# Performance work log

Hardware: AMD Instinct MI355X
Metric: run time of the kernel (lower is better)

## Reference

```python
import jax, jax.numpy as jnp
import numpy as np

HEADS = 8
DIM_HEAD = 64
SCALE = DIM_HEAD ** -0.5


def setup_inputs() -> dict:
    key = jax.random.key(0)
    ks = jax.random.split(key, 6)
    b, n, d_model = 16, 1024, 512
    inner = HEADS * DIM_HEAD  # 512
    std = d_model ** -0.5
    return {
        "x": jax.random.normal(ks[0], (b, n, d_model), jnp.float32),
        "Wq": jax.random.normal(ks[1], (inner, d_model), jnp.float32) * std,
        "Wk": jax.random.normal(ks[2], (inner, d_model), jnp.float32) * std,
        "Wv": jax.random.normal(ks[3], (inner, d_model), jnp.float32) * std,
        "rel_bias": jax.random.normal(ks[4], (HEADS, n, n), jnp.float32) * 0.02,
        "Wo": jax.random.normal(ks[5], (d_model, inner), jnp.float32) * std,
        "bo": jnp.zeros((d_model,), jnp.float32),
    }


def reference(x, Wq, Wk, Wv, rel_bias, Wo, bo):
    b, n, _ = x.shape
    # projections (Linear with weight of shape [out, in], no bias)
    def proj_heads(W):
        t = jnp.einsum('bnc,ec->bne', x, W)             # [b, n, inner]
        return t.reshape(b, n, HEADS, DIM_HEAD).transpose(0, 2, 1, 3)  # [b, h, n, d]
    q = proj_heads(Wq)
    k = proj_heads(Wk)
    v = proj_heads(Wv)
    sim = jnp.einsum('bhid,bhjd->bhij', q, k) * SCALE
    sim = sim + rel_bias[None]                          # additive rel-pos bias
    attn = jax.nn.softmax(sim, axis=-1)
    out = jnp.einsum('bhij,bhjd->bhid', attn, v)        # [b, h, n, d]
    out = out.transpose(0, 2, 1, 3).reshape(b, n, HEADS * DIM_HEAD)
    return jnp.einsum('bne,ce->bnc', out, Wo) + bo
```

## Files before the change

### kernel.cpp

```cpp
#include <hip/hip_runtime.h>

typedef unsigned short u16;
typedef short short8 __attribute__((ext_vector_type(8)));
typedef float fx4 __attribute__((ext_vector_type(4)));
typedef u16 u16x4 __attribute__((ext_vector_type(4)));
typedef u16 u16x8 __attribute__((ext_vector_type(8)));


__device__ __forceinline__ u16 f2bf(float f) {
  union { float f; unsigned u; } v; v.f = f;
  unsigned r = (v.u + 0x7fffu + ((v.u >> 16) & 1u)) >> 16;
  return (u16)r;
}
__device__ __forceinline__ float bf2f(u16 u) {
  union { unsigned u; float f; } v; v.u = ((unsigned)u) << 16;
  return v.f;
}
__device__ __forceinline__ void load_lds16(const void* g, void* l) {
  __builtin_amdgcn_global_load_lds((const __attribute__((address_space(1))) void*)g,
                                   (__attribute__((address_space(3))) void*)l, 16, 0, 0);
}
__device__ __forceinline__ int swz(int row, int colb) {
  return (row << 7) | (colb ^ ((row & 7) << 4));
}

__global__ __launch_bounds__(256) void k_convert(
    const float* __restrict__ x, const float* __restrict__ wq, const float* __restrict__ wk,
    const float* __restrict__ wv, const float* __restrict__ wo, const float* __restrict__ bias,
    u16* __restrict__ xb, u16* __restrict__ wqkv, u16* __restrict__ wob, u16* __restrict__ biasb) {
  const int total = 2228224;
  for (int u = blockIdx.x * blockDim.x + threadIdx.x; u < total; u += gridDim.x * blockDim.x) {
    const float* src; u16* dst; int off;
    if (u < 1048576)      { src = x;    dst = xb;            off = u << 3; }
    else if (u < 1081344) { src = wq;   dst = wqkv;          off = (u - 1048576) << 3; }
    else if (u < 1114112) { src = wk;   dst = wqkv + 262144; off = (u - 1081344) << 3; }
    else if (u < 1146880) { src = wv;   dst = wqkv + 524288; off = (u - 1114112) << 3; }
    else if (u < 1179648) { src = wo;   dst = wob;           off = (u - 1146880) << 3; }
    else                  { src = bias; dst = biasb;         off = (u - 1179648) << 3; }
    float4 a = *(const float4*)(src + off);
    float4 b = *(const float4*)(src + off + 4);
    u16x8 o;
    o[0] = f2bf(a.x); o[1] = f2bf(a.y); o[2] = f2bf(a.z); o[3] = f2bf(a.w);
    o[4] = f2bf(b.x); o[5] = f2bf(b.y); o[6] = f2bf(b.z); o[7] = f2bf(b.w);
    *(u16x8*)(dst + off) = o;
  }
}

__device__ __forceinline__ void gemm_core(const u16* __restrict__ A, const u16* __restrict__ Bm,
                                          int mt, int nt, int tid, fx4 acc[4][4],
                                          u16* ldsA, u16* ldsB) {
  const int w = tid >> 6, l = tid & 63;
  const int wr = w >> 1, wc = w & 1;
  const int lr = l & 15, kg = (l >> 4) * 8;
  for (int k0 = 0; k0 < 512; k0 += 32) {
#pragma unroll
    for (int i = 0; i < 2; ++i) {
      int seg = w * 2 + i;
      int idx = seg * 512 + l * 8;
      int row = idx >> 5, col = idx & 31;
      load_lds16(A  + (mt * 128 + row) * 512 + k0 + col, (char*)ldsA + seg * 1024);
      load_lds16(Bm + (nt * 128 + row) * 512 + k0 + col, (char*)ldsB + seg * 1024);
    }
    __syncthreads();
    short8 a[4], b[4];
#pragma unroll
    for (int mi = 0; mi < 4; ++mi) a[mi] = *(const short8*)&ldsA[(wr * 64 + mi * 16 + lr) * 32 + kg];
#pragma unroll
    for (int ni = 0; ni < 4; ++ni) b[ni] = *(const short8*)&ldsB[(wc * 64 + ni * 16 + lr) * 32 + kg];
#pragma unroll
    for (int mi = 0; mi < 4; ++mi)
#pragma unroll
      for (int ni = 0; ni < 4; ++ni)
        acc[mi][ni] = __builtin_amdgcn_mfma_f32_16x16x32_bf16(a[mi], b[ni], acc[mi][ni], 0, 0, 0);
    __syncthreads();
  }
}

__global__ __launch_bounds__(256) void k_proj(const u16* __restrict__ xb, const u16* __restrict__ wqkv,
                                              u16* __restrict__ Qb, u16* __restrict__ Kb,
                                              u16* __restrict__ Vtb) {
  __shared__ u16 ldsA[128 * 32], ldsB[128 * 32];
  int orig = blockIdx.x;
  int wgid = (orig & 7) * 192 + (orig >> 3);
  int mt = wgid / 12, nt = wgid % 12;
  int tid = threadIdx.x;
  fx4 acc[4][4] = {};
  gemm_core(xb, wqkv, mt, nt, tid, acc, ldsA, ldsB);
  const int w = tid >> 6, l = tid & 63, wr = w >> 1, wc = w & 1;
  const int rb = mt * 128 + wr * 64 + ((l >> 4) << 2);
  const int eb = ((nt & 3) << 7) + wc * 64 + (l & 15);
  if (nt < 8) {
    u16* dst = (nt < 4) ? Qb : Kb;
#pragma unroll
    for (int ni = 0; ni < 4; ++ni) {
      int e = eb + ni * 16, hh = e >> 6, d = e & 63;
#pragma unroll
      for (int mi = 0; mi < 4; ++mi)
#pragma unroll
        for (int j = 0; j < 4; ++j) {
          int r = rb + mi * 16 + j, bb = r >> 10, nn = r & 1023;
          dst[(((bb << 3) + hh) * 1024 + nn) * 64 + d] = f2bf(acc[mi][ni][j]);
        }
    }
  } else {
#pragma unroll
    for (int ni = 0; ni < 4; ++ni) {
      int e = eb + ni * 16, hh = e >> 6, d = e & 63;
#pragma unroll
      for (int mi = 0; mi < 4; ++mi) {
        int r0 = rb + mi * 16, bb = r0 >> 10, nn = r0 & 1023;
        u16x4 p;
#pragma unroll
        for (int j = 0; j < 4; ++j) p[j] = f2bf(acc[mi][ni][j]);
        *(u16x4*)&Vtb[(((bb << 3) + hh) * 64 + d) * 1024 + nn] = p;
      }
    }
  }
}

__global__ __launch_bounds__(256) void k_attn(const u16* __restrict__ Qb, const u16* __restrict__ Kb,
                                              const u16* __restrict__ Vtb, const u16* __restrict__ biasb,
                                              u16* __restrict__ Ob) {
  __shared__ u16 ldsK[64 * 64], ldsV[64 * 64], ldsBias[64 * 64];
  __shared__ u16 ldsP[4][16 * 64];
  int orig = blockIdx.x;
  int wgid = (orig & 7) * 256 + (orig >> 3);
  int h = wgid >> 8, bb = (wgid >> 4) & 15, qt = wgid & 15;
  const int tid = threadIdx.x, w = tid >> 6, l = tid & 63;
  const int lr = l & 15, g = l >> 4;
  const int q0 = qt * 64;
  const u16*  Qbh = Qb + (size_t)((bb * 8 + h) * 1024) * 64;
  const char* Kc  = (const char*)(Kb  + (size_t)((bb * 8 + h) * 1024) * 64);
  const char* Vc  = (const char*)(Vtb + (size_t)((bb * 8 + h) * 64) * 1024);
  const char* Bc  = (const char*)biasb + ((size_t)h << 21);
  const int qrow = q0 + w * 16 + lr;
  short8 qf0 = *(const short8*)&Qbh[qrow * 64 + g * 8];
  short8 qf1 = *(const short8*)&Qbh[qrow * 64 + 32 + g * 8];
  float m_r[4], l_r[4];
  fx4 acc_o[4] = {};
#pragma unroll
  for (int j = 0; j < 4; ++j) { m_r[j] = -1e30f; l_r[j] = 0.f; }

  for (int kt = 0; kt < 16; ++kt) {
#pragma unroll
    for (int i = 0; i < 2; ++i) {
      int segb = (w * 2 + i) * 1024;
      int o = segb + l * 16;
      int bs = o ^ (((o >> 7) & 7) << 4);
      int row = bs >> 7, colb = bs & 127;
      load_lds16(Kc + (size_t)(kt * 64 + row) * 128 + colb, (char*)ldsK + segb);
      load_lds16(Vc + (size_t)row * 2048 + kt * 128 + colb, (char*)ldsV + segb);
      load_lds16(Bc + (size_t)(q0 + row) * 2048 + kt * 128 + colb, (char*)ldsBias + segb);
    }
    __syncthreads();
    fx4 s[4];
#pragma unroll
    for (int ct = 0; ct < 4; ++ct) {
      short8 kf0 = *(const short8*)((char*)ldsK + swz(ct * 16 + lr, g * 16));
      short8 kf1 = *(const short8*)((char*)ldsK + swz(ct * 16 + lr, 64 + g * 16));
      fx4 t = {};
      t = __builtin_amdgcn_mfma_f32_16x16x32_bf16(qf0, kf0, t, 0, 0, 0);
      t = __builtin_amdgcn_mfma_f32_16x16x32_bf16(qf1, kf1, t, 0, 0, 0);
      s[ct] = t;
    }
#pragma unroll
    for (int ct = 0; ct < 4; ++ct)
#pragma unroll
      for (int j = 0; j < 4; ++j) {
        u16 bv = *(const u16*)((char*)ldsBias + swz(w * 16 + g * 4 + j, (ct * 16 + lr) * 2));
        s[ct][j] = s[ct][j] * 0.125f + bf2f(bv);
      }
#pragma unroll
    for (int j = 0; j < 4; ++j) {
      float tm = fmaxf(fmaxf(s[0][j], s[1][j]), fmaxf(s[2][j], s[3][j]));
#pragma unroll
      for (int d = 1; d < 16; d <<= 1) tm = fmaxf(tm, __shfl_xor(tm, d));
      float mn = fmaxf(m_r[j], tm);
      float corr = __expf(m_r[j] - mn);
      m_r[j] = mn;
      float rs = 0.f;
#pragma unroll
      for (int ct = 0; ct < 4; ++ct) { float p = __expf(s[ct][j] - mn); s[ct][j] = p; rs += p; }
#pragma unroll
      for (int d = 1; d < 16; d <<= 1) rs += __shfl_xor(rs, d);
      l_r[j] = l_r[j] * corr + rs;
#pragma unroll
      for (int dt = 0; dt < 4; ++dt) acc_o[dt][j] *= corr;
    }
    char* Pw = (char*)ldsP[w];
#pragma unroll
    for (int ct = 0; ct < 4; ++ct)
#pragma unroll
      for (int j = 0; j < 4; ++j)
        *(u16*)(Pw + swz(g * 4 + j, (ct * 16 + lr) * 2)) = f2bf(s[ct][j]);
    __syncthreads();
    short8 pf0 = *(const short8*)(Pw + swz(lr, g * 16));
    short8 pf1 = *(const short8*)(Pw + swz(lr, 64 + g * 16));
#pragma unroll
    for (int dt = 0; dt < 4; ++dt) {
      short8 vf0 = *(const short8*)((char*)ldsV + swz(dt * 16 + lr, g * 16));
      short8 vf1 = *(const short8*)((char*)ldsV + swz(dt * 16 + lr, 64 + g * 16));
      acc_o[dt] = __builtin_amdgcn_mfma_f32_16x16x32_bf16(pf0, vf0, acc_o[dt], 0, 0, 0);
      acc_o[dt] = __builtin_amdgcn_mfma_f32_16x16x32_bf16(pf1, vf1, acc_o[dt], 0, 0, 0);
    }
    __syncthreads();
  }
#pragma unroll
  for (int j = 0; j < 4; ++j) {
    float inv = 1.f / l_r[j];
    int q = q0 + w * 16 + g * 4 + j;
#pragma unroll
    for (int dt = 0; dt < 4; ++dt) {
      int col = h * 64 + dt * 16 + lr;
      Ob[(size_t)(bb * 1024 + q) * 512 + col] = f2bf(acc_o[dt][j] * inv);
    }
  }
}

__global__ __launch_bounds__(256) void k_out(const u16* __restrict__ Ob, const u16* __restrict__ Wob,
                                             const float* __restrict__ bo, float* __restrict__ out) {
  __shared__ u16 ldsA[128 * 32], ldsB[128 * 32];
  int orig = blockIdx.x;
  int wgid = (orig & 7) * 64 + (orig >> 3);
  int mt = wgid >> 2, nt = wgid & 3;
  int tid = threadIdx.x;
  fx4 acc[4][4] = {};
  gemm_core(Ob, Wob, mt, nt, tid, acc, ldsA, ldsB);
  const int w = tid >> 6, l = tid & 63, wr = w >> 1, wc = w & 1;
  const int rb = mt * 128 + wr * 64 + ((l >> 4) << 2);
  const int eb = nt * 128 + wc * 64 + (l & 15);
#pragma unroll
  for (int ni = 0; ni < 4; ++ni) {
    int e = eb + ni * 16;
    float bv = bo[e];
#pragma unroll
    for (int mi = 0; mi < 4; ++mi)
#pragma unroll
      for (int j = 0; j < 4; ++j) {
        int r = rb + mi * 16 + j;
        out[(size_t)r * 512 + e] = acc[mi][ni][j] + bv;
      }
  }
}

extern "C" void kernel_launch(void* const* d_in, const int* in_sizes, int n_in,
                              void* d_out, int out_size, void* d_ws, size_t ws_size,
                              hipStream_t stream) {
  const float* x    = (const float*)d_in[0];
  const float* wq   = (const float*)d_in[1];
  const float* wk   = (const float*)d_in[2];
  const float* wv   = (const float*)d_in[3];
  const float* bias = (const float*)d_in[4];
  const float* wo   = (const float*)d_in[5];
  const float* bo   = (const float*)d_in[6];
  float* out = (float*)d_out;
  char* ws = (char*)d_ws;
  u16* xb    = (u16*)(ws + 0);
  u16* wqkv  = (u16*)(ws + 16777216);
  u16* wob   = (u16*)(ws + 18350080);
  u16* biasb = (u16*)(ws + 18874368);
  u16* Qb    = (u16*)(ws + 35651584);
  u16* Kb    = (u16*)(ws + 52428800);
  u16* Vtb   = (u16*)(ws + 69206016);
  u16* Ob    = (u16*)(ws + 85983232);

  hipLaunchKernelGGL(k_convert, dim3(2048), dim3(256), 0, stream,
                     x, wq, wk, wv, wo, bias, xb, wqkv, wob, biasb);
  hipLaunchKernelGGL(k_proj, dim3(1536), dim3(256), 0, stream, xb, wqkv, Qb, Kb, Vtb);
  hipLaunchKernelGGL(k_attn, dim3(2048), dim3(256), 0, stream, Qb, Kb, Vtb, biasb, Ob);
  hipLaunchKernelGGL(k_out, dim3(512), dim3(256), 0, stream, Ob, wob, bo, out);
}
```

Before: 303.0 us.

## Double-buffer K/V tiles in attention and load bias directly into registers

The attention kernel now double-buffers the K and V tiles in LDS, issuing the next tile's async global-to-LDS loads before computing on the current tile. Explicit vmcnt waits and raw s_barrier calls replace the per-iteration __syncthreads. The bias tile no longer goes through LDS: each lane reads its 16 bias values straight from global memory into registers. The __syncthreads between the per-wave P write and its read back is removed, relying on P being private to each wave. The aim is to hide load latency and cut LDS traffic and barriers, at the cost of more LDS for buffers and uncoalesced 2-byte global bias loads.

Measured after the change: 282.7 us. -6.7%, faster.

```diff
diff --git a/kernel.cpp b/kernel.cpp
--- a/kernel.cpp
+++ b/kernel.cpp
@@ -121,7 +121,7 @@
 __global__ __launch_bounds__(256) void k_attn(const u16* __restrict__ Qb, const u16* __restrict__ Kb,
                                               const u16* __restrict__ Vtb, const u16* __restrict__ biasb,
                                               u16* __restrict__ Ob) {
-  __shared__ u16 ldsK[64 * 64], ldsV[64 * 64], ldsBias[64 * 64];
+  __shared__ u16 ldsK[2][64 * 64], ldsV[2][64 * 64];
   __shared__ u16 ldsP[4][16 * 64];
   int orig = blockIdx.x;
   int wgid = (orig & 7) * 256 + (orig >> 3);
@@ -132,7 +132,7 @@
   const u16*  Qbh = Qb + (size_t)((bb * 8 + h) * 1024) * 64;
   const char* Kc  = (const char*)(Kb  + (size_t)((bb * 8 + h) * 1024) * 64);
   const char* Vc  = (const char*)(Vtb + (size_t)((bb * 8 + h) * 64) * 1024);
-  const char* Bc  = (const char*)biasb + ((size_t)h << 21);
+  const u16* Bt = biasb + ((size_t)h << 20) + (size_t)(q0 + w * 16 + g * 4) * 1024 + lr;
   const int qrow = q0 + w * 16 + lr;
   short8 qf0 = *(const short8*)&Qbh[qrow * 64 + g * 8];
   short8 qf1 = *(const short8*)&Qbh[qrow * 64 + 32 + g * 8];
@@ -141,23 +141,46 @@
 #pragma unroll
   for (int j = 0; j < 4; ++j) { m_r[j] = -1e30f; l_r[j] = 0.f; }
 
+  const int segb0 = (w * 2) * 1024, segb1 = (w * 2 + 1) * 1024;
+  int o0 = segb0 + l * 16, o1 = segb1 + l * 16;
+  int bs0 = o0 ^ (((o0 >> 7) & 7) << 4), bs1 = o1 ^ (((o1 >> 7) & 7) << 4);
+  int row0 = bs0 >> 7, colb0 = bs0 & 127;
+  int row1 = bs1 >> 7, colb1 = bs1 & 127;
+
+#define STAGE(kt, p)                                                                 \
+  {                                                                                  \
+    load_lds16(Kc + (size_t)((kt) * 64 + row0) * 128 + colb0, (char*)ldsK[p] + segb0); \
+    load_lds16(Vc + (size_t)row0 * 2048 + (kt) * 128 + colb0, (char*)ldsV[p] + segb0); \
+    load_lds16(Kc + (size_t)((kt) * 64 + row1) * 128 + colb1, (char*)ldsK[p] + segb1); \
+    load_lds16(Vc + (size_t)row1 * 2048 + (kt) * 128 + colb1, (char*)ldsV[p] + segb1); \
+  }
+
+  STAGE(0, 0);
+
   for (int kt = 0; kt < 16; ++kt) {
-#pragma unroll
-    for (int i = 0; i < 2; ++i) {
-      int segb = (w * 2 + i) * 1024;
-      int o = segb + l * 16;
-      int bs = o ^ (((o >> 7) & 7) << 4);
-      int row = bs >> 7, colb = bs & 127;
-      load_lds16(Kc + (size_t)(kt * 64 + row) * 128 + colb, (char*)ldsK + segb);
-      load_lds16(Vc + (size_t)row * 2048 + kt * 128 + colb, (char*)ldsV + segb);
-      load_lds16(Bc + (size_t)(q0 + row) * 2048 + kt * 128 + colb, (char*)ldsBias + segb);
-    }
-    __syncthreads();
+    const int p = kt & 1;
+    u16 br[16];
+#pragma unroll
+    for (int ct = 0; ct < 4; ++ct)
+#pragma unroll
+      for (int j = 0; j < 4; ++j)
+        br[ct * 4 + j] = Bt[(size_t)j * 1024 + kt * 64 + ct * 16];
+    __builtin_amdgcn_sched_barrier(0);
+    if (kt < 15) {
+      STAGE(kt + 1, p ^ 1);
+      __builtin_amdgcn_sched_barrier(0);
+      asm volatile("s_waitcnt vmcnt(4)" ::: "memory");
+    } else {
+      asm volatile("s_waitcnt vmcnt(0)" ::: "memory");
+    }
+    __builtin_amdgcn_sched_barrier(0);
+    __builtin_amdgcn_s_barrier();
+
     fx4 s[4];
 #pragma unroll
     for (int ct = 0; ct < 4; ++ct) {
-      short8 kf0 = *(const short8*)((char*)ldsK + swz(ct * 16 + lr, g * 16));
-      short8 kf1 = *(const short8*)((char*)ldsK + swz(ct * 16 + lr, 64 + g * 16));
+      short8 kf0 = *(const short8*)((char*)ldsK[p] + swz(ct * 16 + lr, g * 16));
+      short8 kf1 = *(const short8*)((char*)ldsK[p] + swz(ct * 16 + lr, 64 + g * 16));
       fx4 t = {};
       t = __builtin_amdgcn_mfma_f32_16x16x32_bf16(qf0, kf0, t, 0, 0, 0);
       t = __builtin_amdgcn_mfma_f32_16x16x32_bf16(qf1, kf1, t, 0, 0, 0);
@@ -166,10 +189,8 @@
 #pragma unroll
     for (int ct = 0; ct < 4; ++ct)
 #pragma unroll
-      for (int j = 0; j < 4; ++j) {
-        u16 bv = *(const u16*)((char*)ldsBias + swz(w * 16 + g * 4 + j, (ct * 16 + lr) * 2));
-        s[ct][j] = s[ct][j] * 0.125f + bf2f(bv);
-      }
+      for (int j = 0; j < 4; ++j)
+        s[ct][j] = s[ct][j] * 0.125f + bf2f(br[ct * 4 + j]);
 #pragma unroll
     for (int j = 0; j < 4; ++j) {
       float tm = fmaxf(fmaxf(s[0][j], s[1][j]), fmaxf(s[2][j], s[3][j]));
@@ -180,7 +201,7 @@
       m_r[j] = mn;
       float rs = 0.f;
 #pragma unroll
-      for (int ct = 0; ct < 4; ++ct) { float p = __expf(s[ct][j] - mn); s[ct][j] = p; rs += p; }
+      for (int ct = 0; ct < 4; ++ct) { float p2 = __expf(s[ct][j] - mn); s[ct][j] = p2; rs += p2; }
 #pragma unroll
       for (int d = 1; d < 16; d <<= 1) rs += __shfl_xor(rs, d);
       l_r[j] = l_r[j] * corr + rs;
@@ -193,18 +214,18 @@
 #pragma unroll
       for (int j = 0; j < 4; ++j)
         *(u16*)(Pw + swz(g * 4 + j, (ct * 16 + lr) * 2)) = f2bf(s[ct][j]);
-    __syncthreads();
     short8 pf0 = *(const short8*)(Pw + swz(lr, g * 16));
     short8 pf1 = *(const short8*)(Pw + swz(lr, 64 + g * 16));
 #pragma unroll
     for (int dt = 0; dt < 4; ++dt) {
-      short8 vf0 = *(const short8*)((char*)ldsV + swz(dt * 16 + lr, g * 16));
-      short8 vf1 = *(const short8*)((char*)ldsV + swz(dt * 16 + lr, 64 + g * 16));
+      short8 vf0 = *(const short8*)((char*)ldsV[p] + swz(dt * 16 + lr, g * 16));
+      short8 vf1 = *(const short8*)((char*)ldsV[p] + swz(dt * 16 + lr, 64 + g * 16));
       acc_o[dt] = __builtin_amdgcn_mfma_f32_16x16x32_bf16(pf0, vf0, acc_o[dt], 0, 0, 0);
       acc_o[dt] = __builtin_amdgcn_mfma_f32_16x16x32_bf16(pf1, vf1, acc_o[dt], 0, 0, 0);
     }
-    __syncthreads();
-  }
+    __builtin_amdgcn_s_barrier();
+  }
+#undef STAGE
 #pragma unroll
   for (int j = 0; j < 4; ++j) {
     float inv = 1.f / l_r[j];
```
